# Performance work log

Hardware: AMD Instinct MI355X
Metric: run time of the kernel (lower is better)

## Reference

```python
import jax, jax.numpy as jnp
import numpy as np
import math

ORDER = 7
VAR_SIZE = ORDER + 1
ROW_SIZE = 2048
BATCH = 2048
DIM = 64
COL_SIZE = 16384


def setup_inputs() -> dict:
    key = jax.random.key(0)
    k0, k1, k2, k3, k4, k5, k6 = jax.random.split(key, 7)
    events = jax.random.randint(k0, (ROW_SIZE, BATCH), 0, 2, dtype=jnp.int32)
    col_indices = jax.random.randint(k1, (BATCH,), 0, COL_SIZE, dtype=jnp.int32)
    col_times = jax.random.uniform(k2, (BATCH,), dtype=jnp.float32)
    z_rows = jax.random.uniform(k3, (VAR_SIZE, ROW_SIZE, DIM), dtype=jnp.float32)
    z_cols = jax.random.uniform(k4, (COL_SIZE, DIM), dtype=jnp.float32)
    gamma_rows = jax.random.uniform(k5, (ROW_SIZE,), dtype=jnp.float32)
    gamma_cols = jax.random.uniform(k6, (COL_SIZE,), dtype=jnp.float32)
    return {"events": events, "col_indices": col_indices, "col_times": col_times,
            "z_rows": z_rows, "z_cols": z_cols,
            "gamma_rows": gamma_rows, "gamma_cols": gamma_cols}


def reference(events, col_indices, col_times, z_rows, z_cols, gamma_rows, gamma_cols):
    O = z_rows.shape[0]  # var_size = order + 1
    inv_fact = jnp.asarray([1.0 / math.factorial(o) for o in range(O)], dtype=z_rows.dtype)
    # T[o, b] = t_b^o / o!  (Taylor basis per column time)
    tpow = jnp.power(col_times[None, :], jnp.arange(O, dtype=col_times.dtype)[:, None]) * inv_fact[:, None]
    # Time-varying row positions: z_t[b, n, d] = sum_o z_rows[o, n, d] * T[o, b]
    z_t = jnp.einsum('ond,ob->bnd', z_rows, tpow)
    # Pairwise L2 distance to the matched column embedding (cdist with a single col per time)
    diff = z_t - z_cols[col_indices][:, None, :]            # [B, N, D]
    dist = jnp.sqrt(jnp.sum(diff * diff, axis=-1))          # [B, N]
    logits = gamma_rows[None, :] + gamma_cols[col_indices][:, None] - dist  # [B, N]
    p = jax.nn.sigmoid(logits)
    e = events.T.astype(p.dtype)                            # [B, N]
    # p_mat = p if event else (1 - p)
    p_mat = 1.0 - e - (1.0 - 2.0 * e) * p
    return -jnp.sum(jnp.log(p_mat))
```

## Files before the change

kernel.cpp:

```cpp
#include <hip/hip_runtime.h>
#include <math.h>
#include <stdint.h>

#define NR    2048
#define NB    2048
#define DIMD  64
#define KC    576
#define BK    64
#define KSTEP 9

typedef __bf16 bf16x8 __attribute__((ext_vector_type(8)));
typedef float  f32x4  __attribute__((ext_vector_type(4)));

typedef const __attribute__((address_space(1))) void* gas_p;
typedef __attribute__((address_space(3))) void*       las_p;

__device__ __forceinline__ unsigned short f2bf(float f) {
    unsigned int u = __float_as_uint(f);
    unsigned int r = u + 0x7FFFu + ((u >> 16) & 1u);
    return (unsigned short)(r >> 16);
}

__global__ __launch_bounds__(256) void prep_all(
    const int*   __restrict__ col_indices,
    const float* __restrict__ col_times,
    const float* __restrict__ z_cols,
    const float* __restrict__ gamma_cols,
    const float* __restrict__ z_rows,
    unsigned short* __restrict__ Abuf,
    unsigned short* __restrict__ Bbuf,
    float* __restrict__ cc, float* __restrict__ gcg)
{
    const int tid = threadIdx.x, w = tid >> 6, lane = tid & 63;
    if (blockIdx.x < 512) {
        __shared__ float Tl[4][8];
        const int b  = blockIdx.x * 4 + w;
        const float t  = col_times[b];
        const int   ci = col_indices[b];
        if (lane < 8) {
            float v = 1.f;
            for (int i = 1; i <= lane; ++i) v = v * t / (float)i;
            Tl[w][lane] = v;
        }
        __syncthreads();
        const float cd = z_cols[ci * DIMD + lane];
        unsigned short* arow = Abuf + (size_t)b * KC;
#pragma unroll
        for (int o = 0; o < 8; ++o)
            arow[o * 64 + lane] = f2bf(-2.f * Tl[w][o] * cd);
        arow[512 + lane] = f2bf(Tl[w][lane >> 3] * Tl[w][lane & 7]);
        float s = cd * cd;
#pragma unroll
        for (int m = 1; m < 64; m <<= 1) s += __shfl_xor(s, m, 64);
        if (lane == 0) { cc[b] = s; gcg[b] = gamma_cols[ci]; }
    } else {
        const int n = (blockIdx.x - 512) * 4 + w;
        float z8[8];
#pragma unroll
        for (int o = 0; o < 8; ++o)
            z8[o] = z_rows[o * (NR * DIMD) + n * DIMD + lane];
        unsigned short* brow = Bbuf + (size_t)n * KC;
#pragma unroll
        for (int o = 0; o < 8; ++o)
            brow[o * 64 + lane] = f2bf(z8[o]);
        float myG = 0.f;
#pragma unroll
        for (int o1 = 0; o1 < 8; ++o1)
#pragma unroll
            for (int o2 = o1; o2 < 8; ++o2) {
                float p = z8[o1] * z8[o2];
#pragma unroll
                for (int m = 1; m < 64; m <<= 1) p += __shfl_xor(p, m, 64);
                if (lane == o1 * 8 + o2) myG = p;
                if (o1 != o2 && lane == o2 * 8 + o1) myG = p;
            }
        brow[512 + lane] = f2bf(myG);
    }
}

__global__ __launch_bounds__(256, 2) void p2v_gemm(
    const unsigned short* __restrict__ Abuf,
    const unsigned short* __restrict__ Bbuf,
    const float* __restrict__ cc,
    const float* __restrict__ gcg,
    const float* __restrict__ gamma_rows,
    const int*   __restrict__ events,
    float*       __restrict__ out)
{
    __shared__ unsigned short As[128 * BK] __attribute__((aligned(16)));
    __shared__ unsigned short Bs[64 * BK]  __attribute__((aligned(16)));
    __shared__ float warr[4];

    const int tid = threadIdx.x, w = tid >> 6, lane = tid & 63;
    const int wm = w >> 1, wn = w & 1;
    const int n0 = blockIdx.x * 64, b0 = blockIdx.y * 128;

    const int lr8 = lane >> 3;
    const int cx  = (lane & 7) ^ lr8;
    const size_t gA = (size_t)(b0 + w * 32 + lr8) * KC + cx * 8;
    const size_t gB = (size_t)(n0 + w * 16 + lr8) * KC + cx * 8;
    unsigned short* dA = &As[(w * 32) * BK];
    unsigned short* dB = &Bs[(w * 16) * BK];

    f32x4 acc[4][2];
#pragma unroll
    for (int mi = 0; mi < 4; ++mi)
#pragma unroll
        for (int ni = 0; ni < 2; ++ni) acc[mi][ni] = (f32x4)(0.f);

    for (int ks = 0; ks < KSTEP; ++ks) {
        const int ko = ks * BK;
#pragma unroll
        for (int i = 0; i < 4; ++i)
            __builtin_amdgcn_global_load_lds((gas_p)(Abuf + gA + (size_t)(i * 8) * KC + ko),
                                             (las_p)(dA + i * 512), 16, 0, 0);
#pragma unroll
        for (int i = 0; i < 2; ++i)
            __builtin_amdgcn_global_load_lds((gas_p)(Bbuf + gB + (size_t)(i * 8) * KC + ko),
                                             (las_p)(dB + i * 512), 16, 0, 0);
        __syncthreads();
#pragma unroll
        for (int kk = 0; kk < 2; ++kk) {
            const int slot = (kk * 4 + (lane >> 4)) ^ (lane & 7);
            bf16x8 af[4], bfr[2];
#pragma unroll
            for (int mi = 0; mi < 4; ++mi)
                af[mi] = *reinterpret_cast<const bf16x8*>(
                    &As[(wm * 64 + mi * 16 + (lane & 15)) * BK + slot * 8]);
#pragma unroll
            for (int ni = 0; ni < 2; ++ni)
                bfr[ni] = *reinterpret_cast<const bf16x8*>(
                    &Bs[(wn * 32 + ni * 16 + (lane & 15)) * BK + slot * 8]);
#pragma unroll
            for (int mi = 0; mi < 4; ++mi)
#pragma unroll
                for (int ni = 0; ni < 2; ++ni)
                    acc[mi][ni] = __builtin_amdgcn_mfma_f32_16x16x32_bf16(
                        af[mi], bfr[ni], acc[mi][ni], 0, 0, 0);
        }
        __syncthreads();
    }

    float ls = 0.f;
#pragma unroll
    for (int ni = 0; ni < 2; ++ni) {
        const int n = n0 + wn * 32 + ni * 16 + (lane & 15);
        const float grn = gamma_rows[n];
        const size_t erow = (size_t)n * NB;
#pragma unroll
        for (int mi = 0; mi < 4; ++mi) {
            const int bb = b0 + wm * 64 + mi * 16 + (lane >> 4) * 4;
            const int4   ev  = *reinterpret_cast<const int4*>(&events[erow + bb]);
            const float4 ccv = *reinterpret_cast<const float4*>(&cc[bb]);
            const float4 gcv = *reinterpret_cast<const float4*>(&gcg[bb]);
#define EPJ(cmp, evv)                                                      \
            {                                                              \
                const float d2   = acc[mi][ni].cmp + ccv.cmp;              \
                const float dist = sqrtf(fmaxf(d2, 0.f));                  \
                const float L    = grn + gcv.cmp - dist;                   \
                const float x    = (evv != 0) ? -L : L;                    \
                ls += fmaxf(x, 0.f) + __logf(1.f + __expf(-fabsf(x)));     \
            }
            EPJ(x, ev.x) EPJ(y, ev.y) EPJ(z, ev.z) EPJ(w, ev.w)
#undef EPJ
        }
    }
#pragma unroll
    for (int m = 1; m < 64; m <<= 1) ls += __shfl_xor(ls, m, 64);
    if (lane == 0) warr[w] = ls;
    __syncthreads();
    if (tid == 0) atomicAdd(out, warr[0] + warr[1] + warr[2] + warr[3]);
}

extern "C" void kernel_launch(void* const* d_in, const int* in_sizes, int n_in,
                              void* d_out, int out_size, void* d_ws, size_t ws_size,
                              hipStream_t stream) {
    const int*   events      = (const int*)  d_in[0];
    const int*   col_indices = (const int*)  d_in[1];
    const float* col_times   = (const float*)d_in[2];
    const float* z_rows      = (const float*)d_in[3];
    const float* z_cols      = (const float*)d_in[4];
    const float* gamma_rows  = (const float*)d_in[5];
    const float* gamma_cols  = (const float*)d_in[6];
    float*       out         = (float*)d_out;

    unsigned short* Abuf = (unsigned short*)d_ws;
    unsigned short* Bbuf = Abuf + (size_t)NB * KC;
    float*          cc   = (float*)(Bbuf + (size_t)NR * KC);
    float*          gcg  = cc + NB;

    hipMemsetAsync(out, 0, sizeof(float) * out_size, stream);
    prep_all<<<1024, 256, 0, stream>>>(col_indices, col_times, z_cols, gamma_cols,
                                       z_rows, Abuf, Bbuf, cc, gcg);
    dim3 grid(NR / 64, NB / 128);
    p2v_gemm<<<grid, 256, 0, stream>>>(Abuf, Bbuf, cc, gcg, gamma_rows, events, out);
}
```

Before: 100.2 us.

## Double-buffer GEMM LDS tiles and fold output zeroing into prep kernel

The GEMM kernel now keeps two LDS buffers for the A and B tiles and issues the async global-to-LDS loads for the next K step before computing on the current one. This is meant to hide global-load latency behind the MFMA work. LDS use doubles, which could limit how many blocks fit per CU. Separately, the hipMemsetAsync of the output is replaced by one thread in the prep kernel writing zero, which removes a separate memset operation from the stream.

```diff
diff --git a/kernel.cpp b/kernel.cpp
--- a/kernel.cpp
+++ b/kernel.cpp
@@ -29,9 +29,11 @@
     const float* __restrict__ z_rows,
     unsigned short* __restrict__ Abuf,
     unsigned short* __restrict__ Bbuf,
-    float* __restrict__ cc, float* __restrict__ gcg)
+    float* __restrict__ cc, float* __restrict__ gcg,
+    float* __restrict__ out)
 {
     const int tid = threadIdx.x, w = tid >> 6, lane = tid & 63;
+    if (blockIdx.x == 0 && tid == 0) *out = 0.f;
     if (blockIdx.x < 512) {
         __shared__ float Tl[4][8];
         const int b  = blockIdx.x * 4 + w;
@@ -87,8 +89,8 @@
     const int*   __restrict__ events,
     float*       __restrict__ out)
 {
-    __shared__ unsigned short As[128 * BK] __attribute__((aligned(16)));
-    __shared__ unsigned short Bs[64 * BK]  __attribute__((aligned(16)));
+    __shared__ unsigned short As[2][128 * BK] __attribute__((aligned(16)));
+    __shared__ unsigned short Bs[2][64 * BK]  __attribute__((aligned(16)));
     __shared__ float warr[4];
 
     const int tid = threadIdx.x, w = tid >> 6, lane = tid & 63;
@@ -99,8 +101,8 @@
     const int cx  = (lane & 7) ^ lr8;
     const size_t gA = (size_t)(b0 + w * 32 + lr8) * KC + cx * 8;
     const size_t gB = (size_t)(n0 + w * 16 + lr8) * KC + cx * 8;
-    unsigned short* dA = &As[(w * 32) * BK];
-    unsigned short* dB = &Bs[(w * 16) * BK];
+    const int dAo = (w * 32) * BK;
+    const int dBo = (w * 16) * BK;
 
     f32x4 acc[4][2];
 #pragma unroll
@@ -108,17 +110,28 @@
 #pragma unroll
         for (int ni = 0; ni < 2; ++ni) acc[mi][ni] = (f32x4)(0.f);
 
+#define STAGE(buf, ks)                                                         \
+    {                                                                          \
+        const int ko_ = (ks) * BK;                                             \
+        _Pragma("unroll")                                                      \
+        for (int i = 0; i < 4; ++i)                                            \
+            __builtin_amdgcn_global_load_lds(                                  \
+                (gas_p)(Abuf + gA + (size_t)(i * 8) * KC + ko_),               \
+                (las_p)&As[buf][dAo + i * 512], 16, 0, 0);                     \
+        _Pragma("unroll")                                                      \
+        for (int i = 0; i < 2; ++i)                                            \
+            __builtin_amdgcn_global_load_lds(                                  \
+                (gas_p)(Bbuf + gB + (size_t)(i * 8) * KC + ko_),               \
+                (las_p)&Bs[buf][dBo + i * 512], 16, 0, 0);                     \
+    }
+
+    STAGE(0, 0);
+    __syncthreads();
+
+#pragma unroll
     for (int ks = 0; ks < KSTEP; ++ks) {
-        const int ko = ks * BK;
-#pragma unroll
-        for (int i = 0; i < 4; ++i)
-            __builtin_amdgcn_global_load_lds((gas_p)(Abuf + gA + (size_t)(i * 8) * KC + ko),
-                                             (las_p)(dA + i * 512), 16, 0, 0);
-#pragma unroll
-        for (int i = 0; i < 2; ++i)
-            __builtin_amdgcn_global_load_lds((gas_p)(Bbuf + gB + (size_t)(i * 8) * KC + ko),
-                                             (las_p)(dB + i * 512), 16, 0, 0);
-        __syncthreads();
+        const int cur = ks & 1;
+        if (ks + 1 < KSTEP) STAGE(cur ^ 1, ks + 1);
 #pragma unroll
         for (int kk = 0; kk < 2; ++kk) {
             const int slot = (kk * 4 + (lane >> 4)) ^ (lane & 7);
@@ -126,11 +139,11 @@
 #pragma unroll
             for (int mi = 0; mi < 4; ++mi)
                 af[mi] = *reinterpret_cast<const bf16x8*>(
-                    &As[(wm * 64 + mi * 16 + (lane & 15)) * BK + slot * 8]);
+                    &As[cur][(wm * 64 + mi * 16 + (lane & 15)) * BK + slot * 8]);
 #pragma unroll
             for (int ni = 0; ni < 2; ++ni)
                 bfr[ni] = *reinterpret_cast<const bf16x8*>(
-                    &Bs[(wn * 32 + ni * 16 + (lane & 15)) * BK + slot * 8]);
+                    &Bs[cur][(wn * 32 + ni * 16 + (lane & 15)) * BK + slot * 8]);
 #pragma unroll
             for (int mi = 0; mi < 4; ++mi)
 #pragma unroll
@@ -140,6 +153,7 @@
         }
         __syncthreads();
     }
+#undef STAGE
 
     float ls = 0.f;
 #pragma unroll
@@ -189,9 +203,8 @@
     float*          cc   = (float*)(Bbuf + (size_t)NR * KC);
     float*          gcg  = cc + NB;
 
-    hipMemsetAsync(out, 0, sizeof(float) * out_size, stream);
     prep_all<<<1024, 256, 0, stream>>>(col_indices, col_times, z_cols, gamma_cols,
-                                       z_rows, Abuf, Bbuf, cc, gcg);
+                                       z_rows, Abuf, Bbuf, cc, gcg, out);
     dim3 grid(NR / 64, NB / 128);
     p2v_gemm<<<grid, 256, 0, stream>>>(Abuf, Bbuf, cc, gcg, gamma_rows, events, out);
 }
```

New measurement: 99.74 us (median of 2 runs). Within noise of the previous version (-0.5%).
